# Performance work log

Hardware: AMD Instinct MI355X
Metric: run time of the kernel (lower is better)

## Reference

```python
import jax, jax.numpy as jnp
import numpy as np

B_BOUND = 3.0
K = 10
SCALE_DIM = 8
TOTAL_DIM = 16
HID = 50
N = 262144
TD = TOTAL_DIM - SCALE_DIM  # transform_dim


def setup_inputs() -> dict:
    key = jax.random.key(0)
    ks = jax.random.split(key, 7)
    s = 0.1  # small init so softmax/softplus params stay well-conditioned
    return {
        "x": jax.random.normal(ks[0], (N, TOTAL_DIM), dtype=jnp.float32),
        "w0": s * jax.random.normal(ks[1], (SCALE_DIM, HID), dtype=jnp.float32),
        "b0": jnp.zeros((HID,), jnp.float32),
        "w1": s * jax.random.normal(ks[2], (HID, HID), dtype=jnp.float32),
        "b1": jnp.zeros((HID,), jnp.float32),
        "ww": s * jax.random.normal(ks[3], (HID, TD * K), dtype=jnp.float32),
        "bw": jnp.zeros((TD * K,), jnp.float32),
        "wh": s * jax.random.normal(ks[4], (HID, TD * K), dtype=jnp.float32),
        "bh": jnp.zeros((TD * K,), jnp.float32),
        "wd": s * jax.random.normal(ks[5], (HID, TD * (K - 1)), dtype=jnp.float32),
        "bd": jnp.zeros((TD * (K - 1),), jnp.float32),
    }


def _spline_forward(x, w0, b0, w1, b1, ww, bw, wh, bh, wd, bd):
    B = B_BOUND
    zd = x[:, :SCALE_DIM]          # conditioner input [N, d]
    u = x[:, SCALE_DIM:]           # values to transform [N, D]
    n, D = u.shape

    h = jnp.tanh(zd @ w0 + b0)
    h = jnp.tanh(h @ w1 + b1)

    theta_w = jax.nn.softmax((2.0 * B * (h @ ww + bw)).reshape(n, D, K), axis=-1)
    theta_h = jax.nn.softmax((2.0 * B * (h @ wh + bh)).reshape(n, D, K), axis=-1)
    theta_d = jax.nn.softplus((h @ wd + bd).reshape(n, D, K - 1))

    # Bin edges in [-B, B] via cumsum of normalized widths/heights
    xe = jnp.concatenate(
        [jnp.full((n, D, 1), -B, u.dtype), -B + 2.0 * B * jnp.cumsum(theta_w, axis=-1)], axis=-1)  # [n,D,K+1]
    ye = jnp.concatenate(
        [jnp.full((n, D, 1), -B, u.dtype), -B + 2.0 * B * jnp.cumsum(theta_h, axis=-1)], axis=-1)
    # Knot derivatives: boundary derivatives fixed to 1 (linear tails)
    ones = jnp.ones((n, D, 1), u.dtype)
    d = jnp.concatenate([ones, theta_d, ones], axis=-1)  # [n,D,K+1]

    widths = xe[..., 1:] - xe[..., :-1]
    heights = ye[..., 1:] - ye[..., :-1]

    inside = (u > -B) & (u < B)
    uc = jnp.clip(u, -B, B)
    # per-element bin search
    idx = jnp.clip(jnp.sum((uc[..., None] >= xe[..., :-1]).astype(jnp.int32), axis=-1) - 1, 0, K - 1)
    idx = idx[..., None]
    take = lambda a: jnp.take_along_axis(a, idx, axis=-1)[..., 0]

    xk, yk = take(xe[..., :-1]), take(ye[..., :-1])
    wk, hk = take(widths), take(heights)
    dk, dk1 = take(d[..., :-1]), take(d[..., 1:])

    sk = hk / wk
    xi = (uc - xk) / wk
    om = 1.0 - xi
    denom = sk + (dk1 + dk - 2.0 * sk) * xi * om
    y = yk + hk * (sk * xi * xi + dk * xi * om) / denom
    logdet = 2.0 * jnp.log(sk) + jnp.log(dk1 * xi * xi + 2.0 * sk * xi * om + dk * om * om) - 2.0 * jnp.log(denom)

    zD = jnp.where(inside, y, u)
    ld = jnp.where(inside, logdet, 0.0)
    return jnp.concatenate([zd, zD], axis=1), jnp.sum(ld)


def reference(x, w0, b0, w1, b1, ww, bw, wh, bh, wd, bd):
    return _spline_forward(x, w0, b0, w1, b1, ww, bw, wh, bh, wd, bd)
```

## Files before the change

### kernel.cpp

```cpp
#include <hip/hip_runtime.h>

#define NROWS 262144
#define KK 10
#define BB 3.0f
#define SROW 260
#define SEGF16 (16 * SROW)
#define SENT 0.54132485f

typedef _Float16 v8h __attribute__((ext_vector_type(8)));
typedef _Float16 v4h __attribute__((ext_vector_type(4)));
typedef float v4f __attribute__((ext_vector_type(4)));

#define W0_OFF 0
#define W1_OFF 256
#define WC_OFF 768
#define FRAG_TOTAL 2816
#define SLOTS_OFF (FRAG_TOTAL * 4)

__device__ __forceinline__ float fast_tanh(float a) {
    float e = __expf(2.0f * a);
    return 1.0f - __fdividef(2.0f, e + 1.0f);
}

__device__ __forceinline__ float softplus1(float v) {
    return fmaxf(v, 0.0f) + __logf(1.0f + __expf(-fabsf(v)));
}

__device__ __forceinline__ void spline_task(
    const _Float16* __restrict__ sg, int base, float ud, int g, int d,
    float* __restrict__ out, float& ldacc)
{
    float vals[32];
    #pragma unroll
    for (int blk = 0; blk < 8; ++blk) {
        const v4h p = *(const v4h*)&sg[base + blk * 4];
        vals[4 * blk + 0] = (float)p[0];
        vals[4 * blk + 1] = (float)p[1];
        vals[4 * blk + 2] = (float)p[2];
        vals[4 * blk + 3] = (float)p[3];
    }

    float mw = vals[0];
    #pragma unroll
    for (int i = 1; i < KK; ++i) mw = fmaxf(mw, vals[i]);
    float sw = 0.0f;
    #pragma unroll
    for (int i = 0; i < KK; ++i) { vals[i] = __expf(6.0f * (vals[i] - mw)); sw += vals[i]; }
    const float invw = __fdividef(1.0f, sw);

    float mh = vals[10];
    #pragma unroll
    for (int i = 1; i < KK; ++i) mh = fmaxf(mh, vals[10 + i]);
    float sh = 0.0f;
    #pragma unroll
    for (int i = 0; i < KK; ++i) { vals[10 + i] = __expf(6.0f * (vals[10 + i] - mh)); sh += vals[10 + i]; }
    const float invh = __fdividef(1.0f, sh);

    const float uc = fminf(fmaxf(ud, -BB), BB);
    const bool inside = (ud > -BB) && (ud < BB);

    float cw = 0.0f, ch = 0.0f;
    float xprev = -BB, yprev = -BB, rprev = SENT;
    float xk = -BB, yk = -BB, wk = 1.0f, hk2 = 1.0f, rdk = SENT, rdk1 = SENT;
    #pragma unroll
    for (int i = 0; i < KK; ++i) {
        cw += vals[i] * invw;
        ch += vals[10 + i] * invh;
        const float xnext = fmaf(6.0f, cw, -BB);
        const float ynext = fmaf(6.0f, ch, -BB);
        const float rnext = (i == KK - 1) ? SENT : vals[20 + i];
        const bool c = (i == 0) || (uc >= xprev);
        if (c) { xk = xprev; yk = yprev; wk = xnext - xprev; hk2 = ynext - yprev; rdk = rprev; rdk1 = rnext; }
        xprev = xnext; yprev = ynext; rprev = rnext;
    }
    const float dk = softplus1(rdk);
    const float dk1 = softplus1(rdk1);

    const float rwk = __fdividef(1.0f, wk);
    const float sk = hk2 * rwk;
    const float xi = (uc - xk) * rwk;
    const float om = 1.0f - xi;
    const float denom = sk + (dk1 + dk - 2.0f * sk) * xi * om;
    const float rden = __fdividef(1.0f, denom);
    const float ynum = sk * xi * xi + dk * xi * om;
    const float yv = yk + hk2 * ynum * rden;
    const float larg = dk1 * xi * xi + 2.0f * sk * xi * om + dk * om * om;
    const float ldet = __logf(sk * sk * larg * rden * rden);

    out[g * 16 + 8 + d] = inside ? yv : ud;
    ldacc += inside ? ldet : 0.0f;
}

__global__ __launch_bounds__(256) void nsf_prep(
    const float* __restrict__ w0, const float* __restrict__ b0,
    const float* __restrict__ w1, const float* __restrict__ b1,
    const float* __restrict__ ww, const float* __restrict__ bw,
    const float* __restrict__ wh, const float* __restrict__ bh,
    const float* __restrict__ wd, const float* __restrict__ bd,
    v8h* __restrict__ wsv, float* __restrict__ wsf)
{
    const int t = blockIdx.x * 256 + threadIdx.x;
    if (t < 64) wsf[SLOTS_OFF + t] = 0.0f;
    if (t >= FRAG_TOTAL) return;

    v8h v;
    #pragma unroll
    for (int j = 0; j < 8; ++j) v[j] = (_Float16)0.0f;

    if (t < W1_OFF) {
        const int tile = t >> 6, lane = t & 63, q = lane >> 4, n = tile * 16 + (lane & 15);
        if (n < 50) {
            #pragma unroll
            for (int j = 0; j < 8; ++j) {
                const int k = q * 8 + j;
                if (k < 8)       v[j] = (_Float16)w0[k * 50 + n];
                else if (k == 8) v[j] = (_Float16)b0[n];
            }
        }
    } else if (t < WC_OFF) {
        int p = t - W1_OFF;
        const int step = p >> 8; p &= 255;
        const int tile = p >> 6, lane = p & 63, q = lane >> 4, n = tile * 16 + (lane & 15);
        if (n < 50) {
            #pragma unroll
            for (int j = 0; j < 8; ++j) {
                const int k = step * 32 + q * 8 + j;
                if (k < 50)       v[j] = (_Float16)w1[k * 50 + n];
                else if (k == 50) v[j] = (_Float16)b1[n];
            }
        }
    } else {
        int p = t - WC_OFF;
        const int step = p >> 10; p &= 1023;
        const int tile = p >> 6, lane = p & 63, q = lane >> 4;
        const int cp = tile * 16 + (lane & 15);
        const int d = cp >> 5, jj = cp & 31;
        #pragma unroll
        for (int j = 0; j < 8; ++j) {
            const int k = step * 32 + q * 8 + j;
            float val = 0.0f;
            if (k < 50) {
                if (jj < 10)      val = ww[k * 80 + d * 10 + jj];
                else if (jj < 20) val = wh[k * 80 + d * 10 + (jj - 10)];
                else if (jj < 29) val = wd[k * 72 + d * 9 + (jj - 20)];
            } else if (k == 50) {
                if (jj < 10)      val = bw[d * 10 + jj];
                else if (jj < 20) val = bh[d * 10 + (jj - 10)];
                else if (jj < 29) val = bd[d * 9 + (jj - 20)];
            }
            v[j] = (_Float16)val;
        }
    }
    wsv[t] = v;
}

__global__ __launch_bounds__(64, 2) void nsf_main(
    const float* __restrict__ x,
    const v8h* __restrict__ wsv,
    float* __restrict__ out, float* __restrict__ slots)
{
    __shared__ __align__(16) _Float16 smem[2 * SEGF16];
    const int lane = threadIdx.x & 63;
    const int q = lane >> 4, l15 = lane & 15;
    _Float16* segA = &smem[0];
    _Float16* segB = &smem[SEGF16];
    const int R0 = blockIdx.x * 32;

    const float4* xv = (const float4*)x;
    float4* ov = (float4*)out;

    const float uA0 = x[(R0 + l15) * 16 + 8 + q];
    const float uA1 = x[(R0 + l15) * 16 + 12 + q];
    const float uB0 = x[(R0 + 16 + l15) * 16 + 8 + q];
    const float uB1 = x[(R0 + 16 + l15) * 16 + 12 + q];

    {
        const int gg = R0 + (lane >> 1);
        const int part = lane & 1;
        ov[gg * 4 + part] = xv[gg * 4 + part];
    }

    v8h aA, aB;
    #pragma unroll
    for (int j = 0; j < 8; ++j) { aA[j] = (_Float16)0.0f; aB[j] = (_Float16)0.0f; }
    if (lane < 16) {
        const float4 f0 = xv[(R0 + lane) * 4 + 0];
        const float4 f1 = xv[(R0 + lane) * 4 + 1];
        aA[0] = (_Float16)f0.x; aA[1] = (_Float16)f0.y; aA[2] = (_Float16)f0.z; aA[3] = (_Float16)f0.w;
        aA[4] = (_Float16)f1.x; aA[5] = (_Float16)f1.y; aA[6] = (_Float16)f1.z; aA[7] = (_Float16)f1.w;
        const float4 g0 = xv[(R0 + 16 + lane) * 4 + 0];
        const float4 g1 = xv[(R0 + 16 + lane) * 4 + 1];
        aB[0] = (_Float16)g0.x; aB[1] = (_Float16)g0.y; aB[2] = (_Float16)g0.z; aB[3] = (_Float16)g0.w;
        aB[4] = (_Float16)g1.x; aB[5] = (_Float16)g1.y; aB[6] = (_Float16)g1.z; aB[7] = (_Float16)g1.w;
    }
    if (q == 1) { aA[0] = (_Float16)1.0f; aB[0] = (_Float16)1.0f; }

    #pragma unroll
    for (int t = 0; t < 4; ++t) {
        const v8h b = wsv[W0_OFF + t * 64 + lane];
        v4f cA = __builtin_amdgcn_mfma_f32_16x16x32_f16(aA, b, (v4f)(0.0f), 0, 0, 0);
        v4f cB = __builtin_amdgcn_mfma_f32_16x16x32_f16(aB, b, (v4f)(0.0f), 0, 0, 0);
        const int n = t * 16 + l15;
        #pragma unroll
        for (int rg = 0; rg < 4; ++rg) {
            segA[(q * 4 + rg) * 72 + n] = (_Float16)fast_tanh(cA[rg]);
            segB[(q * 4 + rg) * 72 + n] = (_Float16)fast_tanh(cB[rg]);
        }
    }

    v8h A0A, A1A, A0B, A1B;
    {
        A0A = *(const v8h*)&segA[l15 * 72 + q * 8];
        A1A = *(const v8h*)&segA[l15 * 72 + 32 + q * 8];
        A0B = *(const v8h*)&segB[l15 * 72 + q * 8];
        A1B = *(const v8h*)&segB[l15 * 72 + 32 + q * 8];
        if (q == 2) { A1A[2] = (_Float16)1.0f; A1B[2] = (_Float16)1.0f; }
        #pragma unroll
        for (int t = 0; t < 4; ++t) {
            const v8h bf0 = wsv[W1_OFF + t * 64 + lane];
            const v8h bf1 = wsv[W1_OFF + 256 + t * 64 + lane];
            v4f cA = __builtin_amdgcn_mfma_f32_16x16x32_f16(A0A, bf0, (v4f)(0.0f), 0, 0, 0);
            cA = __builtin_amdgcn_mfma_f32_16x16x32_f16(A1A, bf1, cA, 0, 0, 0);
            v4f cB = __builtin_amdgcn_mfma_f32_16x16x32_f16(A0B, bf0, (v4f)(0.0f), 0, 0, 0);
            cB = __builtin_amdgcn_mfma_f32_16x16x32_f16(A1B, bf1, cB, 0, 0, 0);
            const int n = t * 16 + l15;
            #pragma unroll
            for (int rg = 0; rg < 4; ++rg) {
                segA[(q * 4 + rg) * 72 + n] = (_Float16)fast_tanh(cA[rg]);
                segB[(q * 4 + rg) * 72 + n] = (_Float16)fast_tanh(cB[rg]);
            }
        }
    }

    A0A = *(const v8h*)&segA[l15 * 72 + q * 8];
    A1A = *(const v8h*)&segA[l15 * 72 + 32 + q * 8];
    A0B = *(const v8h*)&segB[l15 * 72 + q * 8];
    A1B = *(const v8h*)&segB[l15 * 72 + 32 + q * 8];
    if (q == 2) { A1A[2] = (_Float16)1.0f; A1B[2] = (_Float16)1.0f; }

    float ldacc = 0.0f;

    #pragma unroll 2
    for (int t = 0; t < 8; ++t) {
        const v8h bf0 = wsv[WC_OFF + t * 64 + lane];
        const v8h bf1 = wsv[WC_OFF + 1024 + t * 64 + lane];
        v4f cA = __builtin_amdgcn_mfma_f32_16x16x32_f16(A0A, bf0, (v4f)(0.0f), 0, 0, 0);
        cA = __builtin_amdgcn_mfma_f32_16x16x32_f16(A1A, bf1, cA, 0, 0, 0);
        v4f cB = __builtin_amdgcn_mfma_f32_16x16x32_f16(A0B, bf0, (v4f)(0.0f), 0, 0, 0);
        cB = __builtin_amdgcn_mfma_f32_16x16x32_f16(A1B, bf1, cB, 0, 0, 0);
        const int cp = t * 16 + l15;
        #pragma unroll
        for (int rg = 0; rg < 4; ++rg) {
            segA[(q * 4 + rg) * SROW + cp] = (_Float16)cA[rg];
            segB[(q * 4 + rg) * SROW + cp] = (_Float16)cB[rg];
        }
    }

    spline_task(segA, l15 * SROW + q * 32, uA0, R0 + l15, q, out, ldacc);
    spline_task(segB, l15 * SROW + q * 32, uB0, R0 + 16 + l15, q, out, ldacc);

    #pragma unroll 2
    for (int t = 8; t < 16; ++t) {
        const v8h bf0 = wsv[WC_OFF + t * 64 + lane];
        const v8h bf1 = wsv[WC_OFF + 1024 + t * 64 + lane];
        v4f cA = __builtin_amdgcn_mfma_f32_16x16x32_f16(A0A, bf0, (v4f)(0.0f), 0, 0, 0);
        cA = __builtin_amdgcn_mfma_f32_16x16x32_f16(A1A, bf1, cA, 0, 0, 0);
        v4f cB = __builtin_amdgcn_mfma_f32_16x16x32_f16(A0B, bf0, (v4f)(0.0f), 0, 0, 0);
        cB = __builtin_amdgcn_mfma_f32_16x16x32_f16(A1B, bf1, cB, 0, 0, 0);
        const int cp = t * 16 + l15;
        #pragma unroll
        for (int rg = 0; rg < 4; ++rg) {
            segA[(q * 4 + rg) * SROW + cp] = (_Float16)cA[rg];
            segB[(q * 4 + rg) * SROW + cp] = (_Float16)cB[rg];
        }
    }

    spline_task(segA, l15 * SROW + (q + 4) * 32, uA1, R0 + l15, q + 4, out, ldacc);
    spline_task(segB, l15 * SROW + (q + 4) * 32, uB1, R0 + 16 + l15, q + 4, out, ldacc);

    #pragma unroll
    for (int off = 32; off > 0; off >>= 1) ldacc += __shfl_down(ldacc, off);
    if (lane == 0) atomicAdd(&slots[blockIdx.x & 63], ldacc);
}

__global__ void nsf_finish(const float* __restrict__ slots, float* __restrict__ ldp) {
    float v = slots[threadIdx.x];
    #pragma unroll
    for (int off = 32; off > 0; off >>= 1) v += __shfl_down(v, off);
    if (threadIdx.x == 0) *ldp = v;
}

extern "C" void kernel_launch(void* const* d_in, const int* in_sizes, int n_in,
                              void* d_out, int out_size, void* d_ws, size_t ws_size,
                              hipStream_t stream) {
    const float* x  = (const float*)d_in[0];
    const float* w0 = (const float*)d_in[1];
    const float* b0 = (const float*)d_in[2];
    const float* w1 = (const float*)d_in[3];
    const float* b1 = (const float*)d_in[4];
    const float* ww = (const float*)d_in[5];
    const float* bw = (const float*)d_in[6];
    const float* wh = (const float*)d_in[7];
    const float* bh = (const float*)d_in[8];
    const float* wd = (const float*)d_in[9];
    const float* bd = (const float*)d_in[10];

    float* out = (float*)d_out;
    float* ldp = out + (size_t)NROWS * 16;
    v8h* wsv = (v8h*)d_ws;
    float* wsf = (float*)d_ws;
    float* slots = wsf + SLOTS_OFF;

    hipLaunchKernelGGL(nsf_prep, dim3((FRAG_TOTAL + 255) / 256), dim3(256), 0, stream,
                       w0, b0, w1, b1, ww, bw, wh, bh, wd, bd, wsv, wsf);
    hipLaunchKernelGGL(nsf_main, dim3(NROWS / 32), dim3(64), 0, stream,
                       x, wsv, out, slots);
    hipLaunchKernelGGL(nsf_finish, dim3(1), dim3(64), 0, stream, slots, ldp);
}
```

Before: 159.3 us.

## Restructure to one 16-row tile per wave, 4 waves/block, fuse final reduction

```diff
diff --git a/kernel.cpp b/kernel.cpp
--- a/kernel.cpp
+++ b/kernel.cpp
@@ -3,9 +3,10 @@
 #define NROWS 262144
 #define KK 10
 #define BB 3.0f
-#define SROW 260
+#define SROW 132
 #define SEGF16 (16 * SROW)
 #define SENT 0.54132485f
+#define TOTAL_WAVES (NROWS / 16)
 
 typedef _Float16 v8h __attribute__((ext_vector_type(8)));
 typedef _Float16 v4h __attribute__((ext_vector_type(4)));
@@ -17,13 +18,28 @@
 #define FRAG_TOTAL 2816
 #define SLOTS_OFF (FRAG_TOTAL * 4)
 
+#if __has_builtin(__builtin_amdgcn_exp2f)
+__device__ __forceinline__ float ex2(float x) { return __builtin_amdgcn_exp2f(x); }
+#else
+__device__ __forceinline__ float ex2(float x) { return __expf(0.6931471805599453f * x); }
+#endif
+#if __has_builtin(__builtin_amdgcn_rcpf)
+__device__ __forceinline__ float frcp(float x) { return __builtin_amdgcn_rcpf(x); }
+#else
+__device__ __forceinline__ float frcp(float x) { return __fdividef(1.0f, x); }
+#endif
+
+#define LOG2E 1.4426950408889634f
+#define C6 (6.0f * LOG2E)
+#define CT (2.0f * LOG2E)
+
 __device__ __forceinline__ float fast_tanh(float a) {
-    float e = __expf(2.0f * a);
-    return 1.0f - __fdividef(2.0f, e + 1.0f);
+    const float e = ex2(CT * a);
+    return fmaf(-2.0f, frcp(e + 1.0f), 1.0f);
 }
 
 __device__ __forceinline__ float softplus1(float v) {
-    return fmaxf(v, 0.0f) + __logf(1.0f + __expf(-fabsf(v)));
+    return fmaxf(v, 0.0f) + __logf(1.0f + ex2(-LOG2E * fabsf(v)));
 }
 
 __device__ __forceinline__ void spline_task(
@@ -43,18 +59,20 @@
     float mw = vals[0];
     #pragma unroll
     for (int i = 1; i < KK; ++i) mw = fmaxf(mw, vals[i]);
+    const float mw8 = mw * C6;
     float sw = 0.0f;
     #pragma unroll
-    for (int i = 0; i < KK; ++i) { vals[i] = __expf(6.0f * (vals[i] - mw)); sw += vals[i]; }
-    const float invw = __fdividef(1.0f, sw);
+    for (int i = 0; i < KK; ++i) { vals[i] = ex2(fmaf(vals[i], C6, -mw8)); sw += vals[i]; }
+    const float invw = frcp(sw);
 
     float mh = vals[10];
     #pragma unroll
     for (int i = 1; i < KK; ++i) mh = fmaxf(mh, vals[10 + i]);
+    const float mh8 = mh * C6;
     float sh = 0.0f;
     #pragma unroll
-    for (int i = 0; i < KK; ++i) { vals[10 + i] = __expf(6.0f * (vals[10 + i] - mh)); sh += vals[10 + i]; }
-    const float invh = __fdividef(1.0f, sh);
+    for (int i = 0; i < KK; ++i) { vals[10 + i] = ex2(fmaf(vals[10 + i], C6, -mh8)); sh += vals[10 + i]; }
+    const float invh = frcp(sh);
 
     const float uc = fminf(fmaxf(ud, -BB), BB);
     const bool inside = (ud > -BB) && (ud < BB);
@@ -76,12 +94,12 @@
     const float dk = softplus1(rdk);
     const float dk1 = softplus1(rdk1);
 
-    const float rwk = __fdividef(1.0f, wk);
+    const float rwk = frcp(wk);
     const float sk = hk2 * rwk;
     const float xi = (uc - xk) * rwk;
     const float om = 1.0f - xi;
     const float denom = sk + (dk1 + dk - 2.0f * sk) * xi * om;
-    const float rden = __fdividef(1.0f, denom);
+    const float rden = frcp(denom);
     const float ynum = sk * xi * xi + dk * xi * om;
     const float yv = yk + hk2 * ynum * rden;
     const float larg = dk1 * xi * xi + 2.0f * sk * xi * om + dk * om * om;
@@ -154,89 +172,70 @@
     wsv[t] = v;
 }
 
-__global__ __launch_bounds__(64, 2) void nsf_main(
+__global__ __launch_bounds__(256, 7) void nsf_main(
     const float* __restrict__ x,
     const v8h* __restrict__ wsv,
     float* __restrict__ out, float* __restrict__ slots)
 {
-    __shared__ __align__(16) _Float16 smem[2 * SEGF16];
+    __shared__ __align__(16) _Float16 smem[4 * SEGF16];
+    const int w = threadIdx.x >> 6;
     const int lane = threadIdx.x & 63;
     const int q = lane >> 4, l15 = lane & 15;
-    _Float16* segA = &smem[0];
-    _Float16* segB = &smem[SEGF16];
-    const int R0 = blockIdx.x * 32;
+    _Float16* seg = &smem[w * SEGF16];
+    const int R0 = (blockIdx.x * 4 + w) * 16;
 
     const float4* xv = (const float4*)x;
-    float4* ov = (float4*)out;
-
-    const float uA0 = x[(R0 + l15) * 16 + 8 + q];
-    const float uA1 = x[(R0 + l15) * 16 + 12 + q];
-    const float uB0 = x[(R0 + 16 + l15) * 16 + 8 + q];
-    const float uB1 = x[(R0 + 16 + l15) * 16 + 12 + q];
+
+    const float u0 = x[(R0 + l15) * 16 + 8 + q];
+    const float u1 = x[(R0 + l15) * 16 + 12 + q];
 
     {
-        const int gg = R0 + (lane >> 1);
-        const int part = lane & 1;
-        ov[gg * 4 + part] = xv[gg * 4 + part];
-    }
-
-    v8h aA, aB;
-    #pragma unroll
-    for (int j = 0; j < 8; ++j) { aA[j] = (_Float16)0.0f; aB[j] = (_Float16)0.0f; }
+        const float2* xv2 = (const float2*)x;
+        float2* ov2 = (float2*)out;
+        const int idx = (R0 + (lane >> 2)) * 8 + (lane & 3);
+        ov2[idx] = xv2[idx];
+    }
+
+    v8h aA;
+    #pragma unroll
+    for (int j = 0; j < 8; ++j) aA[j] = (_Float16)0.0f;
     if (lane < 16) {
         const float4 f0 = xv[(R0 + lane) * 4 + 0];
         const float4 f1 = xv[(R0 + lane) * 4 + 1];
         aA[0] = (_Float16)f0.x; aA[1] = (_Float16)f0.y; aA[2] = (_Float16)f0.z; aA[3] = (_Float16)f0.w;
         aA[4] = (_Float16)f1.x; aA[5] = (_Float16)f1.y; aA[6] = (_Float16)f1.z; aA[7] = (_Float16)f1.w;
-        const float4 g0 = xv[(R0 + 16 + lane) * 4 + 0];
-        const float4 g1 = xv[(R0 + 16 + lane) * 4 + 1];
-        aB[0] = (_Float16)g0.x; aB[1] = (_Float16)g0.y; aB[2] = (_Float16)g0.z; aB[3] = (_Float16)g0.w;
-        aB[4] = (_Float16)g1.x; aB[5] = (_Float16)g1.y; aB[6] = (_Float16)g1.z; aB[7] = (_Float16)g1.w;
-    }
-    if (q == 1) { aA[0] = (_Float16)1.0f; aB[0] = (_Float16)1.0f; }
+    }
+    if (q == 1) aA[0] = (_Float16)1.0f;
 
     #pragma unroll
     for (int t = 0; t < 4; ++t) {
         const v8h b = wsv[W0_OFF + t * 64 + lane];
-        v4f cA = __builtin_amdgcn_mfma_f32_16x16x32_f16(aA, b, (v4f)(0.0f), 0, 0, 0);
-        v4f cB = __builtin_amdgcn_mfma_f32_16x16x32_f16(aB, b, (v4f)(0.0f), 0, 0, 0);
+        v4f c = __builtin_amdgcn_mfma_f32_16x16x32_f16(aA, b, (v4f)(0.0f), 0, 0, 0);
         const int n = t * 16 + l15;
         #pragma unroll
-        for (int rg = 0; rg < 4; ++rg) {
-            segA[(q * 4 + rg) * 72 + n] = (_Float16)fast_tanh(cA[rg]);
-            segB[(q * 4 + rg) * 72 + n] = (_Float16)fast_tanh(cB[rg]);
-        }
-    }
-
-    v8h A0A, A1A, A0B, A1B;
-    {
-        A0A = *(const v8h*)&segA[l15 * 72 + q * 8];
-        A1A = *(const v8h*)&segA[l15 * 72 + 32 + q * 8];
-        A0B = *(const v8h*)&segB[l15 * 72 + q * 8];
-        A1B = *(const v8h*)&segB[l15 * 72 + 32 + q * 8];
-        if (q == 2) { A1A[2] = (_Float16)1.0f; A1B[2] = (_Float16)1.0f; }
-        #pragma unroll
-        for (int t = 0; t < 4; ++t) {
-            const v8h bf0 = wsv[W1_OFF + t * 64 + lane];
-            const v8h bf1 = wsv[W1_OFF + 256 + t * 64 + lane];
-            v4f cA = __builtin_amdgcn_mfma_f32_16x16x32_f16(A0A, bf0, (v4f)(0.0f), 0, 0, 0);
-            cA = __builtin_amdgcn_mfma_f32_16x16x32_f16(A1A, bf1, cA, 0, 0, 0);
-            v4f cB = __builtin_amdgcn_mfma_f32_16x16x32_f16(A0B, bf0, (v4f)(0.0f), 0, 0, 0);
-            cB = __builtin_amdgcn_mfma_f32_16x16x32_f16(A1B, bf1, cB, 0, 0, 0);
-            const int n = t * 16 + l15;
-            #pragma unroll
-            for (int rg = 0; rg < 4; ++rg) {
-                segA[(q * 4 + rg) * 72 + n] = (_Float16)fast_tanh(cA[rg]);
-                segB[(q * 4 + rg) * 72 + n] = (_Float16)fast_tanh(cB[rg]);
-            }
-        }
-    }
-
-    A0A = *(const v8h*)&segA[l15 * 72 + q * 8];
-    A1A = *(const v8h*)&segA[l15 * 72 + 32 + q * 8];
-    A0B = *(const v8h*)&segB[l15 * 72 + q * 8];
-    A1B = *(const v8h*)&segB[l15 * 72 + 32 + q * 8];
-    if (q == 2) { A1A[2] = (_Float16)1.0f; A1B[2] = (_Float16)1.0f; }
+        for (int rg = 0; rg < 4; ++rg)
+            seg[(q * 4 + rg) * 72 + n] = (_Float16)fast_tanh(c[rg]);
+    }
+
+    v8h A0, A1;
+    A0 = *(const v8h*)&seg[l15 * 72 + q * 8];
+    A1 = *(const v8h*)&seg[l15 * 72 + 32 + q * 8];
+    if (q == 2) A1[2] = (_Float16)1.0f;
+    #pragma unroll
+    for (int t = 0; t < 4; ++t) {
+        const v8h bf0 = wsv[W1_OFF + t * 64 + lane];
+        const v8h bf1 = wsv[W1_OFF + 256 + t * 64 + lane];
+        v4f c = __builtin_amdgcn_mfma_f32_16x16x32_f16(A0, bf0, (v4f)(0.0f), 0, 0, 0);
+        c = __builtin_amdgcn_mfma_f32_16x16x32_f16(A1, bf1, c, 0, 0, 0);
+        const int n = t * 16 + l15;
+        #pragma unroll
+        for (int rg = 0; rg < 4; ++rg)
+            seg[(q * 4 + rg) * 72 + n] = (_Float16)fast_tanh(c[rg]);
+    }
+
+    A0 = *(const v8h*)&seg[l15 * 72 + q * 8];
+    A1 = *(const v8h*)&seg[l15 * 72 + 32 + q * 8];
+    if (q == 2) A1[2] = (_Float16)1.0f;
 
     float ldacc = 0.0f;
 
@@ -244,50 +243,44 @@
     for (int t = 0; t < 8; ++t) {
         const v8h bf0 = wsv[WC_OFF + t * 64 + lane];
         const v8h bf1 = wsv[WC_OFF + 1024 + t * 64 + lane];
-        v4f cA = __builtin_amdgcn_mfma_f32_16x16x32_f16(A0A, bf0, (v4f)(0.0f), 0, 0, 0);
-        cA = __builtin_amdgcn_mfma_f32_16x16x32_f16(A1A, bf1, cA, 0, 0, 0);
-        v4f cB = __builtin_amdgcn_mfma_f32_16x16x32_f16(A0B, bf0, (v4f)(0.0f), 0, 0, 0);
-        cB = __builtin_amdgcn_mfma_f32_16x16x32_f16(A1B, bf1, cB, 0, 0, 0);
+        v4f c = __builtin_amdgcn_mfma_f32_16x16x32_f16(A0, bf0, (v4f)(0.0f), 0, 0, 0);
+        c = __builtin_amdgcn_mfma_f32_16x16x32_f16(A1, bf1, c, 0, 0, 0);
         const int cp = t * 16 + l15;
         #pragma unroll
-        for (int rg = 0; rg < 4; ++rg) {
-            segA[(q * 4 + rg) * SROW + cp] = (_Float16)cA[rg];
-            segB[(q * 4 + rg) * SROW + cp] = (_Float16)cB[rg];
-        }
-    }
-
-    spline_task(segA, l15 * SROW + q * 32, uA0, R0 + l15, q, out, ldacc);
-    spline_task(segB, l15 * SROW + q * 32, uB0, R0 + 16 + l15, q, out, ldacc);
+        for (int rg = 0; rg < 4; ++rg)
+            seg[(q * 4 + rg) * SROW + cp] = (_Float16)c[rg];
+    }
+    spline_task(seg, l15 * SROW + q * 32, u0, R0 + l15, q, out, ldacc);
 
     #pragma unroll 2
     for (int t = 8; t < 16; ++t) {
         const v8h bf0 = wsv[WC_OFF + t * 64 + lane];
         const v8h bf1 = wsv[WC_OFF + 1024 + t * 64 + lane];
-        v4f cA = __builtin_amdgcn_mfma_f32_16x16x32_f16(A0A, bf0, (v4f)(0.0f), 0, 0, 0);
-        cA = __builtin_amdgcn_mfma_f32_16x16x32_f16(A1A, bf1, cA, 0, 0, 0);
-        v4f cB = __builtin_amdgcn_mfma_f32_16x16x32_f16(A0B, bf0, (v4f)(0.0f), 0, 0, 0);
-        cB = __builtin_amdgcn_mfma_f32_16x16x32_f16(A1B, bf1, cB, 0, 0, 0);
-        const int cp = t * 16 + l15;
-        #pragma unroll
-        for (int rg = 0; rg < 4; ++rg) {
-            segA[(q * 4 + rg) * SROW + cp] = (_Float16)cA[rg];
-            segB[(q * 4 + rg) * SROW + cp] = (_Float16)cB[rg];
-        }
-    }
-
-    spline_task(segA, l15 * SROW + (q + 4) * 32, uA1, R0 + l15, q + 4, out, ldacc);
-    spline_task(segB, l15 * SROW + (q + 4) * 32, uB1, R0 + 16 + l15, q + 4, out, ldacc);
+        v4f c = __builtin_amdgcn_mfma_f32_16x16x32_f16(A0, bf0, (v4f)(0.0f), 0, 0, 0);
+        c = __builtin_amdgcn_mfma_f32_16x16x32_f16(A1, bf1, c, 0, 0, 0);
+        const int cp = (t - 8) * 16 + l15;
+        #pragma unroll
+        for (int rg = 0; rg < 4; ++rg)
+            seg[(q * 4 + rg) * SROW + cp] = (_Float16)c[rg];
+    }
+    spline_task(seg, l15 * SROW + q * 32, u1, R0 + l15, q + 4, out, ldacc);
 
     #pragma unroll
     for (int off = 32; off > 0; off >>= 1) ldacc += __shfl_down(ldacc, off);
-    if (lane == 0) atomicAdd(&slots[blockIdx.x & 63], ldacc);
-}
-
-__global__ void nsf_finish(const float* __restrict__ slots, float* __restrict__ ldp) {
-    float v = slots[threadIdx.x];
-    #pragma unroll
-    for (int off = 32; off > 0; off >>= 1) v += __shfl_down(v, off);
-    if (threadIdx.x == 0) *ldp = v;
+    int last = 0;
+    if (lane == 0) {
+        atomicAdd(&slots[(blockIdx.x * 4 + w) & 31], ldacc);
+        __threadfence();
+        const unsigned old = atomicAdd((unsigned int*)&slots[63], 1u);
+        last = (old == (unsigned)(TOTAL_WAVES - 1)) ? 1 : 0;
+    }
+    last = __shfl(last, 0);
+    if (last) {
+        float v = (lane < 32) ? atomicAdd(&slots[lane], 0.0f) : 0.0f;
+        #pragma unroll
+        for (int off = 32; off > 0; off >>= 1) v += __shfl_down(v, off);
+        if (lane == 0) out[(size_t)NROWS * 16] = v;
+    }
 }
 
 extern "C" void kernel_launch(void* const* d_in, const int* in_sizes, int n_in,
@@ -306,14 +299,12 @@
     const float* bd = (const float*)d_in[10];
 
     float* out = (float*)d_out;
-    float* ldp = out + (size_t)NROWS * 16;
     v8h* wsv = (v8h*)d_ws;
     float* wsf = (float*)d_ws;
     float* slots = wsf + SLOTS_OFF;
 
     hipLaunchKernelGGL(nsf_prep, dim3((FRAG_TOTAL + 255) / 256), dim3(256), 0, stream,
                        w0, b0, w1, b1, ww, bw, wh, bh, wd, bd, wsv, wsf);
-    hipLaunchKernelGGL(nsf_main, dim3(NROWS / 32), dim3(64), 0, stream,
+    hipLaunchKernelGGL(nsf_main, dim3(NROWS / 64), dim3(256), 0, stream,
                        x, wsv, out, slots);
-    hipLaunchKernelGGL(nsf_finish, dim3(1), dim3(64), 0, stream, slots, ldp);
-}
+}
```

Result: slower. 532.5 us (+234.3%).
